# Kernel optimization log

Measured on AMD Instinct MI355X. Metric: run time of the kernel, lower is better.

The kernel has to match this reference:

```python
import jax, jax.numpy as jnp
import numpy as np

C = 1024   # n_embd = dim_att = dim_k = dim_v
H = 16     # n_head
K = 64     # k_head_size
V = 64     # v_head_size
DF = 2048  # dim_ffn = (2*C)//32*32
B = 4
T = 1024
N_LAYER = 24
LAYER_ID = 12


def setup_inputs() -> dict:
    key = jax.random.key(0)
    ks = jax.random.split(key, 8)
    r01 = LAYER_ID / (N_LAYER - 1)
    r10 = 1.0 - LAYER_ID / N_LAYER
    ddd = (jnp.arange(C, dtype=jnp.float32) / C)[None, None, :]
    maa_x = 1.0 - ddd ** r10
    maa_k = 1.0 - ddd ** r10
    maa_v = 1.0 - (ddd ** r10 + 0.3 * r01)
    maa_r = 1.0 - ddd ** (0.5 * r10)
    n = jnp.arange(C, dtype=jnp.float32)
    zigzag = ((jnp.arange(C) + 1) % 3 - 1).astype(jnp.float32) * 0.1
    u = (r01 * (1.0 - n / (C - 1)) + zigzag).reshape(H, K)
    # LoRA mats: torch init is zeros / uniform(-0.01,0.01); use small uniform for both
    # so the token-shift LoRA path is actually exercised.
    w1 = jax.random.uniform(ks[0], (C, 96), minval=-0.01, maxval=0.01)
    w2 = jax.random.uniform(ks[1], (3, 32, C), minval=-0.01, maxval=0.01)
    s = 0.02
    Wr = jax.random.normal(ks[2], (C, C)) * s
    Wk = jax.random.normal(ks[3], (C, C)) * s
    Wvg = jax.random.normal(ks[4], (C, 2 * (C + DF))) * s
    Wo = jax.random.normal(ks[5], (C + DF, C)) * s
    ln_g = jnp.ones((C,), jnp.float32)
    ln_b = jnp.zeros((C,), jnp.float32)
    x = jax.random.normal(ks[6], (B, T, C), dtype=jnp.float32)
    return dict(x=x, maa_x=maa_x, maa_k=maa_k, maa_v=maa_v, maa_r=maa_r,
                w1=w1, w2=w2, u=u, Wr=Wr, Wk=Wk, Wvg=Wvg, Wo=Wo,
                ln_g=ln_g, ln_b=ln_b)


def _wkv6(r, k, v, e, u):
    # r,k,e: (B,T,H,K); v: (B,T,H,V); u: (H,K). Decayed linear-attention scan.
    rt = r.transpose(1, 0, 2, 3)
    kt = k.transpose(1, 0, 2, 3)
    vt = v.transpose(1, 0, 2, 3)
    et = e.transpose(1, 0, 2, 3)

    def step(S, inp):  # S: (B,H,K,V)
        r_t, k_t, v_t, e_t = inp
        kv = k_t[..., :, None] * v_t[..., None, :]           # (B,H,K,V)
        out = jnp.einsum('bhk,bhkv->bhv', r_t, S + u[None, :, :, None] * kv)
        return S * e_t[..., :, None] + kv, out

    S0 = jnp.zeros((r.shape[0], u.shape[0], u.shape[1], v.shape[-1]), r.dtype)
    _, o = jax.lax.scan(step, S0, (rt, kt, vt, et))
    return o.transpose(1, 0, 2, 3)  # (B,T,H,V)


def reference(x, maa_x, maa_k, maa_v, maa_r, w1, w2, u, Wr, Wk, Wvg, Wo, ln_g, ln_b):
    Bx, Tx, Cx = x.shape
    # time_shift: ZeroPad2d((0,0,1,-1)) -> shift right by 1 along T with zero pad
    xs = jnp.concatenate([jnp.zeros_like(x[:, :1]), x[:, :-1]], axis=1)
    xx = xs - x
    xxx = x + xx * maa_x
    m = jnp.tanh(xxx @ w1).reshape(Bx, Tx, 3, -1)        # (B,T,3,32)
    m = jnp.einsum('btld,ldc->lbtc', m, w2)              # (3,B,T,C)
    mk, mv, mr = m[0], m[1], m[2]
    xk = x + xx * (maa_k + mk)
    xv = x + xx * (maa_v + mv)
    xr = x + xx * (maa_r + mr)
    r = xr @ Wr
    w = xk @ Wk
    e = jnp.exp(-jnp.exp(w))   # per-channel decay used by the WKV kernel
    k = 1.0 - e                # k = 1 - exp(-exp(w))
    vg = xv @ Wvg
    vffn, gate = jnp.split(vg, 2, axis=-1)
    vffn = vffn * jax.nn.silu(gate)
    v, ffn = vffn[..., :Cx], vffn[..., Cx:]
    o = _wkv6(r.reshape(Bx, Tx, H, K), k.reshape(Bx, Tx, H, K),
              v.reshape(Bx, Tx, H, V), e.reshape(Bx, Tx, H, K), u)
    o = o.reshape(Bx, Tx, Cx)
    mu = o.mean(-1, keepdims=True)
    var = o.var(-1, keepdims=True)
    o = (o - mu) / jnp.sqrt(var + 1e-5) * ln_g + ln_b
    return jnp.concatenate([o, ffn], axis=-1) @ Wo
```

## Files before the change

### kernel.cpp

```cpp
#include <hip/hip_runtime.h>
#include <hip/hip_bf16.h>
#include <math.h>

#define Bn 4
#define Tn 1024
#define Cn 1024
#define Hn 16
#define Kn 64
#define DFn 2048
#define NCn 16
#define Ln 64

typedef __bf16 bf16x8 __attribute__((ext_vector_type(8)));
typedef float f32x4 __attribute__((ext_vector_type(4)));

#define GLD(dst, src) \
  __builtin_amdgcn_global_load_lds((__attribute__((address_space(1))) const void*)(src), \
                                   (__attribute__((address_space(3))) void*)(dst), 16, 0, 0)

__device__ __forceinline__ float rdlane(float v, int l) {
  return __int_as_float(__builtin_amdgcn_readlane(__float_as_int(v), l));
}

__device__ __forceinline__ unsigned short bfbits(float f) {
  union { __hip_bfloat16 h; unsigned short u; } cv;
  cv.h = __float2bfloat16(f);
  return cv.u;
}

__global__ __launch_bounds__(256) void k_prep(const float* __restrict__ x,
                                              const float* __restrict__ maa_x,
                                              float* __restrict__ xx,
                                              __hip_bfloat16* __restrict__ xxx16) {
  int idx = blockIdx.x * 256 + threadIdx.x;
  int c4 = idx & 255;
  int bt = idx >> 8;
  int t = bt & (Tn - 1);
  const float4* x4 = (const float4*)x;
  float4 xv = x4[idx];
  float4 xp;
  if (t > 0) xp = x4[idx - 256];
  else { xp.x = 0.f; xp.y = 0.f; xp.z = 0.f; xp.w = 0.f; }
  float4 d;
  d.x = xp.x - xv.x; d.y = xp.y - xv.y; d.z = xp.z - xv.z; d.w = xp.w - xv.w;
  float4 m = ((const float4*)maa_x)[c4];
  ushort4 o;
  o.x = bfbits(fmaf(d.x, m.x, xv.x));
  o.y = bfbits(fmaf(d.y, m.y, xv.y));
  o.z = bfbits(fmaf(d.z, m.z, xv.z));
  o.w = bfbits(fmaf(d.w, m.w, xv.w));
  ((float4*)xx)[idx] = d;
  ((ushort4*)xxx16)[idx] = o;
}

__global__ __launch_bounds__(256) void k_mix1_16(const __hip_bfloat16* __restrict__ A,
                                                 const __hip_bfloat16* __restrict__ Bt,
                                                 __hip_bfloat16* __restrict__ m1) {
  const int K = 1024;
  __shared__ __align__(16) __hip_bfloat16 Al[128 * 32];
  __shared__ __align__(16) __hip_bfloat16 Bl[96 * 32];
  const int tid = threadIdx.x;
  const int wid = tid >> 6, lane = tid & 63;
  const int wr = wid >> 1, wc = wid & 1;
  const int row0 = blockIdx.x * 128;
  const char* gsrc[4];
  char* ldst[4];
  bool act[4];
  #pragma unroll
  for (int i = 0; i < 4; ++i) {
    const int s = i * 4 + wid;
    act[i] = (s < 14);
    const int ss = act[i] ? s : 0;
    if (ss < 8) {
      const int r = ss * 16 + (lane >> 2);
      gsrc[i] = (const char*)(A + (size_t)(row0 + r) * K) + (lane & 3) * 16;
      ldst[i] = (char*)&Al[0] + ss * 1024;
    } else {
      const int r = (ss - 8) * 16 + (lane >> 2);
      gsrc[i] = (const char*)(Bt + (size_t)r * K) + (lane & 3) * 16;
      ldst[i] = (char*)&Bl[0] + (ss - 8) * 1024;
    }
  }
  f32x4 acc[4][3];
  #pragma unroll
  for (int i = 0; i < 4; ++i)
    #pragma unroll
    for (int j = 0; j < 3; ++j)
      acc[i][j] = (f32x4){0.f, 0.f, 0.f, 0.f};
  const int g = lane >> 4, m = lane & 15;
  for (int k0 = 0; k0 < K; k0 += 32) {
    #pragma unroll
    for (int i = 0; i < 4; ++i) if (act[i]) GLD(ldst[i], gsrc[i]);
    #pragma unroll
    for (int i = 0; i < 4; ++i) gsrc[i] += 64;
    __syncthreads();
    bf16x8 af[4], bfr[3];
    #pragma unroll
    for (int i = 0; i < 4; ++i)
      af[i] = *(const bf16x8*)&Al[(wr * 64 + i * 16 + m) * 32 + g * 8];
    #pragma unroll
    for (int j = 0; j < 3; ++j)
      bfr[j] = *(const bf16x8*)&Bl[(wc * 48 + j * 16 + m) * 32 + g * 8];
    #pragma unroll
    for (int i = 0; i < 4; ++i)
      #pragma unroll
      for (int j = 0; j < 3; ++j)
        acc[i][j] = __builtin_amdgcn_mfma_f32_16x16x32_bf16(af[i], bfr[j], acc[i][j], 0, 0, 0);
    __syncthreads();
  }
  #pragma unroll
  for (int i = 0; i < 4; ++i) {
    const int grow = row0 + wr * 64 + i * 16 + g * 4;
    #pragma unroll
    for (int j = 0; j < 3; ++j) {
      const int gcol = wc * 48 + j * 16 + m;
      #pragma unroll
      for (int e = 0; e < 4; ++e)
        m1[(size_t)(grow + e) * 96 + gcol] = __float2bfloat16(tanhf(acc[i][j][e]));
    }
  }
}

__global__ __launch_bounds__(256) void k_mix2_16(const __hip_bfloat16* __restrict__ m1,
                                                 const __hip_bfloat16* __restrict__ w2t,
                                                 const float* __restrict__ x,
                                                 const float* __restrict__ xx,
                                                 const float* __restrict__ maa_k,
                                                 const float* __restrict__ maa_v,
                                                 const float* __restrict__ maa_r,
                                                 __hip_bfloat16* __restrict__ xk,
                                                 __hip_bfloat16* __restrict__ xv,
                                                 __hip_bfloat16* __restrict__ xr) {
  __shared__ __align__(16) __hip_bfloat16 Al[128 * 96];
  __shared__ __align__(16) __hip_bfloat16 Bl[3 * 64 * 32];
  const int tid = threadIdx.x;
  const int wid = tid >> 6, lane = tid & 63;
  const int wr = wid >> 1, wc = wid & 1;
  const int row0 = blockIdx.y * 128, col0 = blockIdx.x * 64;
  {
    const char* abase = (const char*)(m1 + (size_t)row0 * 96) + lane * 16;
    #pragma unroll
    for (int i = 0; i < 6; ++i) {
      const int s = wid + i * 4;
      GLD((char*)&Al[0] + s * 1024, abase + s * 1024);
    }
  }
  {
    const char* bbase = (const char*)w2t + (size_t)col0 * 64 + lane * 16;
    #pragma unroll
    for (int i = 0; i < 3; ++i) {
      const int s = wid + i * 4;
      const int l = s >> 2, q = s & 3;
      GLD((char*)&Bl[0] + s * 1024, bbase + (size_t)l * 65536 + q * 1024);
    }
  }
  __syncthreads();
  const int g = lane >> 4, m = lane & 15;
  f32x4 a0[4][2], a1[4][2], a2[4][2];
  #pragma unroll
  for (int i = 0; i < 4; ++i)
    #pragma unroll
    for (int j = 0; j < 2; ++j) {
      a0[i][j] = (f32x4){0.f,0.f,0.f,0.f};
      a1[i][j] = (f32x4){0.f,0.f,0.f,0.f};
      a2[i][j] = (f32x4){0.f,0.f,0.f,0.f};
    }
  #pragma unroll
  for (int l = 0; l < 3; ++l) {
    bf16x8 af[4], bfj[2];
    #pragma unroll
    for (int i = 0; i < 4; ++i)
      af[i] = *(const bf16x8*)&Al[(wr * 64 + i * 16 + m) * 96 + l * 32 + g * 8];
    #pragma unroll
    for (int j = 0; j < 2; ++j)
      bfj[j] = *(const bf16x8*)&Bl[(l * 64 + wc * 32 + j * 16 + m) * 32 + g * 8];
    #pragma unroll
    for (int i = 0; i < 4; ++i)
      #pragma unroll
      for (int j = 0; j < 2; ++j) {
        if (l == 0) a0[i][j] = __builtin_amdgcn_mfma_f32_16x16x32_bf16(af[i], bfj[j], a0[i][j], 0, 0, 0);
        if (l == 1) a1[i][j] = __builtin_amdgcn_mfma_f32_16x16x32_bf16(af[i], bfj[j], a1[i][j], 0, 0, 0);
        if (l == 2) a2[i][j] = __builtin_amdgcn_mfma_f32_16x16x32_bf16(af[i], bfj[j], a2[i][j], 0, 0, 0);
      }
  }
  #pragma unroll
  for (int i = 0; i < 4; ++i) {
    const int grow = row0 + wr * 64 + i * 16 + g * 4;
    #pragma unroll
    for (int j = 0; j < 2; ++j) {
      const int gcol = col0 + wc * 32 + j * 16 + m;
      const float mk_ = maa_k[gcol], mv_ = maa_v[gcol], mr_ = maa_r[gcol];
      #pragma unroll
      for (int e = 0; e < 4; ++e) {
        const size_t off = (size_t)(grow + e) * 1024 + gcol;
        const float xval = x[off], xxv = xx[off];
        xk[off] = __float2bfloat16(fmaf(xxv, mk_ + a0[i][j][e], xval));
        xv[off] = __float2bfloat16(fmaf(xxv, mv_ + a1[i][j][e], xval));
        xr[off] = __float2bfloat16(fmaf(xxv, mr_ + a2[i][j][e], xval));
      }
    }
  }
}

__global__ __launch_bounds__(256) void k_cvt_all(const float* __restrict__ w1,
                                                 const float* __restrict__ w2,
                                                 const float* __restrict__ Wr,
                                                 const float* __restrict__ Wk,
                                                 const float* __restrict__ Wvg,
                                                 const float* __restrict__ Wo,
                                                 __hip_bfloat16* __restrict__ w1t,
                                                 __hip_bfloat16* __restrict__ w2t,
                                                 __hip_bfloat16* __restrict__ Wrt,
                                                 __hip_bfloat16* __restrict__ Wkt,
                                                 __hip_bfloat16* __restrict__ Wvgt,
                                                 __hip_bfloat16* __restrict__ Wot) {
  int b = blockIdx.x;
  const float* W; __hip_bfloat16* Wt; int K, N, nx, rel;
  if (b < 96)        { W = w1;  Wt = w1t;  K = 1024; N = 96;   nx = 3;   rel = b; }
  else if (b < 192)  { int l = (b - 96) >> 5; rel = (b - 96) & 31;
                       W = w2 + l * 32768; Wt = w2t + l * 32768; K = 32; N = 1024; nx = 32; }
  else if (b < 1216) { W = Wr;  Wt = Wrt;  K = 1024; N = 1024; nx = 32;  rel = b - 192; }
  else if (b < 2240) { W = Wk;  Wt = Wkt;  K = 1024; N = 1024; nx = 32;  rel = b - 1216; }
  else if (b < 8384) { W = Wvg; Wt = Wvgt; K = 1024; N = 6144; nx = 192; rel = b - 2240; }
  else               { W = Wo;  Wt = Wot;  K = 3072; N = 1024; nx = 32;  rel = b - 8384; }
  int n0 = (rel % nx) * 32, k0 = (rel / nx) * 32;
  __shared__ float tile[32][33];
  int tid = threadIdx.x;
  int c = tid & 31, r = tid >> 5;
  #pragma unroll
  for (int i = 0; i < 4; ++i)
    tile[r + i * 8][c] = W[(size_t)(k0 + r + i * 8) * N + n0 + c];
  __syncthreads();
  #pragma unroll
  for (int i = 0; i < 4; ++i)
    Wt[(size_t)(n0 + r + i * 8) * K + k0 + c] = __float2bfloat16(tile[c][r + i * 8]);
}

template <int FN, int EPI>
__global__ __launch_bounds__(256) void k_gemm16(const __hip_bfloat16* __restrict__ A,
                                                const __hip_bfloat16* __restrict__ Bt,
                                                float* __restrict__ C,
                                                const int K, const int N) {
  constexpr int BN = FN * 32;
  constexpr int NISS = 8 + BN / 16;
  constexpr int PW = NISS / 4;
  __shared__ __align__(16) __hip_bfloat16 Al[128 * 32];
  __shared__ __align__(16) __hip_bfloat16 Bl[BN * 32];
  const int tid = threadIdx.x;
  const int wid = tid >> 6, lane = tid & 63;
  const int wr = wid >> 1, wc = wid & 1;
  const int row0 = blockIdx.y * 128, col0 = blockIdx.x * BN;
  const char* gsrc[PW];
  char* ldst[PW];
  #pragma unroll
  for (int i = 0; i < PW; ++i) {
    const int s = wid + i * 4;
    if (s < 8) {
      const int r = s * 16 + (lane >> 2);
      gsrc[i] = (const char*)(A + (size_t)(row0 + r) * K) + (lane & 3) * 16;
      ldst[i] = (char*)&Al[0] + s * 1024;
    } else {
      const int r = (s - 8) * 16 + (lane >> 2);
      gsrc[i] = (const char*)(Bt + (size_t)(col0 + r) * K) + (lane & 3) * 16;
      ldst[i] = (char*)&Bl[0] + (s - 8) * 1024;
    }
  }
  f32x4 acc[4][FN];
  #pragma unroll
  for (int i = 0; i < 4; ++i)
    #pragma unroll
    for (int j = 0; j < FN; ++j)
      acc[i][j] = (f32x4){0.f, 0.f, 0.f, 0.f};
  const int g = lane >> 4, m = lane & 15;
  for (int k0 = 0; k0 < K; k0 += 32) {
    #pragma unroll
    for (int i = 0; i < PW; ++i) GLD(ldst[i], gsrc[i]);
    #pragma unroll
    for (int i = 0; i < PW; ++i) gsrc[i] += 64;
    __syncthreads();
    bf16x8 af[4], bfr[FN];
    #pragma unroll
    for (int i = 0; i < 4; ++i)
      af[i] = *(const bf16x8*)&Al[(wr * 64 + i * 16 + m) * 32 + g * 8];
    #pragma unroll
    for (int j = 0; j < FN; ++j)
      bfr[j] = *(const bf16x8*)&Bl[(wc * (BN / 2) + j * 16 + m) * 32 + g * 8];
    #pragma unroll
    for (int i = 0; i < 4; ++i)
      #pragma unroll
      for (int j = 0; j < FN; ++j)
        acc[i][j] = __builtin_amdgcn_mfma_f32_16x16x32_bf16(af[i], bfr[j], acc[i][j], 0, 0, 0);
    __syncthreads();
  }
  #pragma unroll
  for (int i = 0; i < 4; ++i) {
    const int grow = row0 + wr * 64 + i * 16 + g * 4;
    #pragma unroll
    for (int j = 0; j < FN; ++j) {
      const int gcol = col0 + wc * (BN / 2) + j * 16 + m;
      #pragma unroll
      for (int e = 0; e < 4; ++e) {
        float val = acc[i][j][e];
        if (EPI == 1) val = expf(-expf(val));
        C[(size_t)(grow + e) * N + gcol] = val;
      }
    }
  }
}

__global__ __launch_bounds__(256) void k_gemm_vg16(const __hip_bfloat16* __restrict__ A,
                                                   const __hip_bfloat16* __restrict__ Bt,
                                                   float* __restrict__ v,
                                                   __hip_bfloat16* __restrict__ ffn) {
  const int K = 1024;
  __shared__ __align__(16) __hip_bfloat16 Al[128 * 32];
  __shared__ __align__(16) __hip_bfloat16 B1l[64 * 32];
  __shared__ __align__(16) __hip_bfloat16 B2l[64 * 32];
  const int tid = threadIdx.x;
  const int wid = tid >> 6, lane = tid & 63;
  const int wr = wid >> 1, wc = wid & 1;
  const int row0 = blockIdx.y * 128, col0 = blockIdx.x * 64;
  const char* gsrc[4];
  char* ldst[4];
  #pragma unroll
  for (int i = 0; i < 4; ++i) {
    const int s = wid + i * 4;
    if (s < 8) {
      const int r = s * 16 + (lane >> 2);
      gsrc[i] = (const char*)(A + (size_t)(row0 + r) * K) + (lane & 3) * 16;
      ldst[i] = (char*)&Al[0] + s * 1024;
    } else if (s < 12) {
      const int r = col0 + (s - 8) * 16 + (lane >> 2);
      gsrc[i] = (const char*)(Bt + (size_t)r * K) + (lane & 3) * 16;
      ldst[i] = (char*)&B1l[0] + (s - 8) * 1024;
    } else {
      const int r = 3072 + col0 + (s - 12) * 16 + (lane >> 2);
      gsrc[i] = (const char*)(Bt + (size_t)r * K) + (lane & 3) * 16;
      ldst[i] = (char*)&B2l[0] + (s - 12) * 1024;
    }
  }
  f32x4 a1[4][2], a2[4][2];
  #pragma unroll
  for (int i = 0; i < 4; ++i)
    #pragma unroll
    for (int j = 0; j < 2; ++j) {
      a1[i][j] = (f32x4){0.f, 0.f, 0.f, 0.f};
      a2[i][j] = (f32x4){0.f, 0.f, 0.f, 0.f};
    }
  const int g = lane >> 4, m = lane & 15;
  for (int k0 = 0; k0 < K; k0 += 32) {
    #pragma unroll
    for (int i = 0; i < 4; ++i) GLD(ldst[i], gsrc[i]);
    #pragma unroll
    for (int i = 0; i < 4; ++i) gsrc[i] += 64;
    __syncthreads();
    bf16x8 af[4], b1f[2], b2f[2];
    #pragma unroll
    for (int i = 0; i < 4; ++i)
      af[i] = *(const bf16x8*)&Al[(wr * 64 + i * 16 + m) * 32 + g * 8];
    #pragma unroll
    for (int j = 0; j < 2; ++j) {
      b1f[j] = *(const bf16x8*)&B1l[(wc * 32 + j * 16 + m) * 32 + g * 8];
      b2f[j] = *(const bf16x8*)&B2l[(wc * 32 + j * 16 + m) * 32 + g * 8];
    }
    #pragma unroll
    for (int i = 0; i < 4; ++i)
      #pragma unroll
      for (int j = 0; j < 2; ++j) {
        a1[i][j] = __builtin_amdgcn_mfma_f32_16x16x32_bf16(af[i], b1f[j], a1[i][j], 0, 0, 0);
        a2[i][j] = __builtin_amdgcn_mfma_f32_16x16x32_bf16(af[i], b2f[j], a2[i][j], 0, 0, 0);
      }
    __syncthreads();
  }
  const bool to_v = (col0 < 1024);
  #pragma unroll
  for (int i = 0; i < 4; ++i) {
    const int grow = row0 + wr * 64 + i * 16 + g * 4;
    #pragma unroll
    for (int j = 0; j < 2; ++j) {
      const int gcol = col0 + wc * 32 + j * 16 + m;
      #pragma unroll
      for (int e = 0; e < 4; ++e) {
        float gate = a2[i][j][e];
        float val = a1[i][j][e] * (gate / (1.f + expf(-gate)));
        if (to_v) v[(size_t)(grow + e) * 1024 + gcol] = val;
        else ffn[(size_t)(grow + e) * 2048 + (gcol - 1024)] = __float2bfloat16(val);
      }
    }
  }
}

__global__ __launch_bounds__(256) void k_gemm_wo16(const __hip_bfloat16* __restrict__ A1,
                                                   const __hip_bfloat16* __restrict__ A2,
                                                   const __hip_bfloat16* __restrict__ Bt,
                                                   float* __restrict__ C) {
  const int Kt = 3072;
  __shared__ __align__(16) __hip_bfloat16 Al[128 * 32];
  __shared__ __align__(16) __hip_bfloat16 Bl[64 * 32];
  const int tid = threadIdx.x;
  const int wid = tid >> 6, lane = tid & 63;
  const int wr = wid >> 1, wc = wid & 1;
  const int row0 = blockIdx.y * 128, col0 = blockIdx.x * 64;
  const char* gsrc[3];
  char* ldst[3];
  #pragma unroll
  for (int i = 0; i < 3; ++i) {
    const int s = wid + i * 4;
    if (s < 8) {
      const int r = s * 16 + (lane >> 2);
      gsrc[i] = (const char*)(A1 + (size_t)(row0 + r) * 1024) + (lane & 3) * 16;
      ldst[i] = (char*)&Al[0] + s * 1024;
    } else {
      const int r = col0 + (s - 8) * 16 + (lane >> 2);
      gsrc[i] = (const char*)(Bt + (size_t)r * Kt) + (lane & 3) * 16;
      ldst[i] = (char*)&Bl[0] + (s - 8) * 1024;
    }
  }
  f32x4 acc[4][2];
  #pragma unroll
  for (int i = 0; i < 4; ++i)
    #pragma unroll
    for (int j = 0; j < 2; ++j)
      acc[i][j] = (f32x4){0.f, 0.f, 0.f, 0.f};
  const int g = lane >> 4, m = lane & 15;

  #define WO_STEP() do {                                                          \
    _Pragma("unroll")                                                             \
    for (int i = 0; i < 3; ++i) GLD(ldst[i], gsrc[i]);                            \
    _Pragma("unroll")                                                             \
    for (int i = 0; i < 3; ++i) gsrc[i] += 64;                                    \
    __syncthreads();                                                              \
    bf16x8 af[4], bfr[2];                                                         \
    _Pragma("unroll")                                                             \
    for (int i = 0; i < 4; ++i)                                                   \
      af[i] = *(const bf16x8*)&Al[(wr * 64 + i * 16 + m) * 32 + g * 8];           \
    _Pragma("unroll")                                                             \
    for (int j = 0; j < 2; ++j)                                                   \
      bfr[j] = *(const bf16x8*)&Bl[(wc * 32 + j * 16 + m) * 32 + g * 8];          \
    _Pragma("unroll")                                                             \
    for (int i = 0; i < 4; ++i)                                                   \
      _Pragma("unroll")                                                           \
      for (int j = 0; j < 2; ++j)                                                 \
        acc[i][j] = __builtin_amdgcn_mfma_f32_16x16x32_bf16(af[i], bfr[j],        \
                                                            acc[i][j], 0, 0, 0); \
    __syncthreads();                                                              \
  } while (0)

  for (int k0 = 0; k0 < 1024; k0 += 32) WO_STEP();
  #pragma unroll
  for (int i = 0; i < 3; ++i) {
    const int s = wid + i * 4;
    if (s < 8) {
      const int r = s * 16 + (lane >> 2);
      gsrc[i] = (const char*)(A2 + (size_t)(row0 + r) * 2048) + (lane & 3) * 16;
    }
  }
  for (int k0 = 0; k0 < 2048; k0 += 32) WO_STEP();
  #undef WO_STEP

  #pragma unroll
  for (int i = 0; i < 4; ++i) {
    const int grow = row0 + wr * 64 + i * 16 + g * 4;
    #pragma unroll
    for (int j = 0; j < 2; ++j) {
      const int gcol = col0 + wc * 32 + j * 16 + m;
      #pragma unroll
      for (int e = 0; e < 4; ++e)
        C[(size_t)(grow + e) * 1024 + gcol] = acc[i][j][e];
    }
  }
}

#define TTn 8
__global__ __launch_bounds__(256) void k_wkv1(const float* __restrict__ r,
                                              const float* __restrict__ e,
                                              const float* __restrict__ v,
                                              const float* __restrict__ u,
                                              float* __restrict__ o,
                                              float* __restrict__ Dcum,
                                              float* __restrict__ Dtot,
                                              float* __restrict__ Inc) {
  int blk = blockIdx.x;
  int c = blk & (NCn - 1);
  int bh = blk >> 4;
  int b = bh >> 4, h = bh & 15;
  int tid = threadIdx.x, wave = tid >> 6, lane = tid & 63;
  size_t base = (size_t)b * Tn * Cn + (size_t)h * 64 + (size_t)c * Ln * Cn;
  int jbase = wave * 16 + (lane & 15);
  float uv = u[h * 64 + jbase];
  float st[16];
  #pragma unroll
  for (int i = 0; i < 16; ++i) st[i] = 0.f;
  float cum = 1.f;
  __shared__ float yp[4][TTn][64];
  for (int tb = 0; tb < Ln / TTn; ++tb) {
    float rv8[TTn], ev8[TTn], vv8[TTn];
    #pragma unroll
    for (int tt = 0; tt < TTn; ++tt) {
      size_t off = base + (size_t)(tb * TTn + tt) * Cn;
      rv8[tt] = r[off + jbase];
      ev8[tt] = e[off + jbase];
      vv8[tt] = v[off + lane];
    }
    float yb[TTn];
    #pragma unroll
    for (int tt = 0; tt < TTn; ++tt) {
      const float rv = rv8[tt], ev = ev8[tt], vv = vv8[tt];
      if (lane < 16)
        Dcum[base + (size_t)(tb * TTn + tt) * Cn + jbase] = cum;
      cum *= ev;
      float p = rv * uv * (1.f - ev);
      p += __shfl_xor(p, 1, 16);
      p += __shfl_xor(p, 2, 16);
      p += __shfl_xor(p, 4, 16);
      p += __shfl_xor(p, 8, 16);
      float y = p * vv;
      #pragma unroll
      for (int jj = 0; jj < 16; ++jj) {
        float rj = rdlane(rv, jj);
        float ej = rdlane(ev, jj);
        float kv = fmaf(-ej, vv, vv);
        y = fmaf(rj, st[jj], y);
        st[jj] = fmaf(st[jj], ej, kv);
      }
      yb[tt] = y;
    }
    #pragma unroll
    for (int tt = 0; tt < TTn; ++tt) yp[wave][tt][lane] = yb[tt];
    __syncthreads();
    #pragma unroll
    for (int q = 0; q < TTn / 4; ++q) {
      int tt = wave * (TTn / 4) + q;
      size_t off = base + (size_t)(tb * TTn + tt) * Cn;
      o[off + lane] = yp[0][tt][lane] + yp[1][tt][lane] + yp[2][tt][lane] + yp[3][tt][lane];
    }
    __syncthreads();
  }
  size_t sbase = ((size_t)bh * NCn + c) * 4096;
  #pragma unroll
  for (int jj = 0; jj < 16; ++jj)
    Inc[sbase + (size_t)(wave * 16 + jj) * 64 + lane] = st[jj];
  if (lane < 16)
    Dtot[((size_t)bh * NCn + c) * 64 + jbase] = cum;
}

__global__ __launch_bounds__(256) void k_wkv2(float* __restrict__ S,
                                              const float* __restrict__ Dtot) {
  int bh = blockIdx.x;
  int tid = threadIdx.x;
  float4 s[4];
  #pragma unroll
  for (int j = 0; j < 4; ++j) { s[j].x = 0.f; s[j].y = 0.f; s[j].z = 0.f; s[j].w = 0.f; }
  size_t sb = (size_t)bh * NCn * 4096;
  for (int c = 0; c < NCn; ++c) {
    float4* entry = (float4*)(S + sb + (size_t)c * 4096);
    const float* dt = Dtot + ((size_t)bh * NCn + c) * 64;
    #pragma unroll
    for (int j = 0; j < 4; ++j) {
      int idx4 = tid + j * 256;
      int k = idx4 >> 4;
      float d = dt[k];
      float4 inc = entry[idx4];
      float4 cur = s[j];
      entry[idx4] = cur;
      s[j].x = fmaf(cur.x, d, inc.x);
      s[j].y = fmaf(cur.y, d, inc.y);
      s[j].z = fmaf(cur.z, d, inc.z);
      s[j].w = fmaf(cur.w, d, inc.w);
    }
  }
}

__global__ __launch_bounds__(256) void k_wkv3(const float* __restrict__ r,
                                              const float* __restrict__ Dcum,
                                              const float* __restrict__ S,
                                              float* __restrict__ o) {
  int blk = blockIdx.x;
  int c = blk & (NCn - 1);
  if (c == 0) return;
  int bh = blk >> 4;
  int b = bh >> 4, h = bh & 15;
  int tid = threadIdx.x, wave = tid >> 6, lane = tid & 63;
  const float* Sg = S + ((size_t)bh * NCn + c) * 4096;
  float sreg[64];
  #pragma unroll
  for (int k = 0; k < 64; ++k) sreg[k] = Sg[k * 64 + lane];
  size_t base = (size_t)b * Tn * Cn + (size_t)h * 64 + (size_t)c * Ln * Cn;
  for (int ti = 0; ti < 16; ++ti) {
    int t = wave * 16 + ti;
    size_t off = base + (size_t)t * Cn;
    float rd = r[off + lane] * Dcum[off + lane];
    float y = 0.f;
    #pragma unroll
    for (int k = 0; k < 64; ++k)
      y = fmaf(rdlane(rd, k), sreg[k], y);
    o[off + lane] += y;
  }
}

__global__ __launch_bounds__(256) void k_ln(const float* __restrict__ o,
                                            const float* __restrict__ g,
                                            const float* __restrict__ bta,
                                            __hip_bfloat16* __restrict__ ln16) {
  int bt = blockIdx.x, tid = threadIdx.x;
  const float4* row = (const float4*)(o + (size_t)bt * 1024);
  float4 v = row[tid];
  float s = v.x + v.y + v.z + v.w;
  float s2 = fmaf(v.x, v.x, fmaf(v.y, v.y, fmaf(v.z, v.z, v.w * v.w)));
  #pragma unroll
  for (int m = 1; m < 64; m <<= 1) {
    s += __shfl_xor(s, m, 64);
    s2 += __shfl_xor(s2, m, 64);
  }
  __shared__ float rs[4], rq[4];
  if ((tid & 63) == 0) { rs[tid >> 6] = s; rq[tid >> 6] = s2; }
  __syncthreads();
  s = rs[0] + rs[1] + rs[2] + rs[3];
  s2 = rq[0] + rq[1] + rq[2] + rq[3];
  float mu = s * (1.f / 1024.f);
  float var = s2 * (1.f / 1024.f) - mu * mu;
  float rstd = rsqrtf(var + 1e-5f);
  float4 gv = ((const float4*)g)[tid];
  float4 bv = ((const float4*)bta)[tid];
  ushort4 outv;
  outv.x = bfbits(fmaf((v.x - mu) * rstd, gv.x, bv.x));
  outv.y = bfbits(fmaf((v.y - mu) * rstd, gv.y, bv.y));
  outv.z = bfbits(fmaf((v.z - mu) * rstd, gv.z, bv.z));
  outv.w = bfbits(fmaf((v.w - mu) * rstd, gv.w, bv.w));
  ((ushort4*)((unsigned short*)ln16 + (size_t)bt * 1024))[tid] = outv;
}

extern "C" void kernel_launch(void* const* d_in, const int* in_sizes, int n_in,
                              void* d_out, int out_size, void* d_ws, size_t ws_size,
                              hipStream_t stream) {
  const float* x     = (const float*)d_in[0];
  const float* maa_x = (const float*)d_in[1];
  const float* maa_k = (const float*)d_in[2];
  const float* maa_v = (const float*)d_in[3];
  const float* maa_r = (const float*)d_in[4];
  const float* w1    = (const float*)d_in[5];
  const float* w2    = (const float*)d_in[6];
  const float* u     = (const float*)d_in[7];
  const float* Wr    = (const float*)d_in[8];
  const float* Wk    = (const float*)d_in[9];
  const float* Wvg   = (const float*)d_in[10];
  const float* Wo    = (const float*)d_in[11];
  const float* ln_g  = (const float*)d_in[12];
  const float* ln_b  = (const float*)d_in[13];
  float* out = (float*)d_out;
  float* ws = (float*)d_ws;

  const size_t M1 = 1048576;
  float* xx    = ws;
  __hip_bfloat16* xxx16 = (__hip_bfloat16*)(ws + 4 * M1);
  __hip_bfloat16* m1_16 = (__hip_bfloat16*)(ws + 8 * M1);
  __hip_bfloat16* w1t = (__hip_bfloat16*)(ws + 8 * M1 + 393216);
  __hip_bfloat16* w2t = (__hip_bfloat16*)(ws + 8 * M1 + 442368);
  __hip_bfloat16* xk16 = (__hip_bfloat16*)(ws + 8 * M1 + 524288);
  __hip_bfloat16* xv16 = (__hip_bfloat16*)(ws + 10 * M1 + 524288);
  __hip_bfloat16* xr16 = (__hip_bfloat16*)(ws + 12 * M1 + 524288);
  float* ee    = ws + 14 * M1 + 524288;
  float* vv    = ws + 18 * M1 + 524288;
  float* Sbuf  = ws + 22 * M1 + 524288;
  __hip_bfloat16* ffn16 = (__hip_bfloat16*)(ws + 26 * M1 + 524288);
  __hip_bfloat16* Wr16t = (__hip_bfloat16*)(ws + 30 * M1 + 524288);
  __hip_bfloat16* Wk16t = (__hip_bfloat16*)(ws + 31 * M1);
  __hip_bfloat16* Wvg16t = (__hip_bfloat16*)(ws + 31 * M1 + 524288);
  __hip_bfloat16* Wo16t = (__hip_bfloat16*)(ws + 34 * M1 + 524288);
  float* rr = ws + 4 * M1;
  float* oo = xx;
  float* Dcum = ws + 8 * M1 + 524288;
  float* Dtot = (float*)m1_16;
  __hip_bfloat16* ln16 = (__hip_bfloat16*)Sbuf;

  k_cvt_all<<<11456, 256, 0, stream>>>(w1, w2, Wr, Wk, Wvg, Wo,
                                       w1t, w2t, Wr16t, Wk16t, Wvg16t, Wo16t);

  k_prep<<<4096, 256, 0, stream>>>(x, maa_x, xx, xxx16);
  k_mix1_16<<<32, 256, 0, stream>>>(xxx16, w1t, m1_16);
  k_mix2_16<<<dim3(16, 32), 256, 0, stream>>>(m1_16, w2t, x, xx, maa_k, maa_v, maa_r,
                                              xk16, xv16, xr16);
  k_gemm16<2, 0><<<dim3(16, 32), 256, 0, stream>>>(xr16, Wr16t, rr, 1024, 1024);
  k_gemm_vg16<<<dim3(48, 32), 256, 0, stream>>>(xv16, Wvg16t, vv, ffn16);
  k_gemm16<2, 1><<<dim3(16, 32), 256, 0, stream>>>(xk16, Wk16t, ee, 1024, 1024);
  k_wkv1<<<64 * NCn, 256, 0, stream>>>(rr, ee, vv, u, oo, Dcum, Dtot, Sbuf);
  k_wkv2<<<64, 256, 0, stream>>>(Sbuf, Dtot);
  k_wkv3<<<64 * NCn, 256, 0, stream>>>(rr, Dcum, Sbuf, oo);
  k_ln<<<4096, 256, 0, stream>>>(oo, ln_g, ln_b, ln16);
  k_gemm_wo16<<<dim3(16, 32), 256, 0, stream>>>(ln16, ffn16, Wo16t, out);
}
```

Measured before the change: 339.0 us.

## Merge Wr/Wk GEMMs into one launch and widen VG GEMM tile to 128 columns

The r and k projection GEMMs are combined into a single kernel launch that uses blockIdx.z to pick the operands and whether to apply the exp(-exp) epilogue. This removes one launch and gives a larger grid of 1024 blocks. The fused value/gate GEMM now uses 128-column tiles instead of 64, so each A tile is reused across twice as many outputs and the grid drops to 768 blocks. The trade-off is more accumulator registers (64 f32x4) and more LDS per block, which may lower occupancy.

```diff
diff --git a/kernel.cpp b/kernel.cpp
--- a/kernel.cpp
+++ b/kernel.cpp
@@ -236,24 +236,27 @@
     Wt[(size_t)(n0 + r + i * 8) * K + k0 + c] = __float2bfloat16(tile[c][r + i * 8]);
 }
 
-template <int FN, int EPI>
-__global__ __launch_bounds__(256) void k_gemm16(const __hip_bfloat16* __restrict__ A,
-                                                const __hip_bfloat16* __restrict__ Bt,
-                                                float* __restrict__ C,
-                                                const int K, const int N) {
-  constexpr int BN = FN * 32;
-  constexpr int NISS = 8 + BN / 16;
-  constexpr int PW = NISS / 4;
+__global__ __launch_bounds__(256) void k_gemm_re(const __hip_bfloat16* __restrict__ Ar,
+                                                 const __hip_bfloat16* __restrict__ Btr,
+                                                 float* __restrict__ Cr,
+                                                 const __hip_bfloat16* __restrict__ Ak,
+                                                 const __hip_bfloat16* __restrict__ Btk,
+                                                 float* __restrict__ Ck) {
+  const int K = 1024, N = 1024;
+  const int z = blockIdx.z;
+  const __hip_bfloat16* A  = z ? Ak : Ar;
+  const __hip_bfloat16* Bt = z ? Btk : Btr;
+  float* C = z ? Ck : Cr;
   __shared__ __align__(16) __hip_bfloat16 Al[128 * 32];
-  __shared__ __align__(16) __hip_bfloat16 Bl[BN * 32];
+  __shared__ __align__(16) __hip_bfloat16 Bl[64 * 32];
   const int tid = threadIdx.x;
   const int wid = tid >> 6, lane = tid & 63;
   const int wr = wid >> 1, wc = wid & 1;
-  const int row0 = blockIdx.y * 128, col0 = blockIdx.x * BN;
-  const char* gsrc[PW];
-  char* ldst[PW];
-  #pragma unroll
-  for (int i = 0; i < PW; ++i) {
+  const int row0 = blockIdx.y * 128, col0 = blockIdx.x * 64;
+  const char* gsrc[3];
+  char* ldst[3];
+  #pragma unroll
+  for (int i = 0; i < 3; ++i) {
     const int s = wid + i * 4;
     if (s < 8) {
       const int r = s * 16 + (lane >> 2);
@@ -265,30 +268,30 @@
       ldst[i] = (char*)&Bl[0] + (s - 8) * 1024;
     }
   }
-  f32x4 acc[4][FN];
+  f32x4 acc[4][2];
   #pragma unroll
   for (int i = 0; i < 4; ++i)
     #pragma unroll
-    for (int j = 0; j < FN; ++j)
+    for (int j = 0; j < 2; ++j)
       acc[i][j] = (f32x4){0.f, 0.f, 0.f, 0.f};
   const int g = lane >> 4, m = lane & 15;
   for (int k0 = 0; k0 < K; k0 += 32) {
     #pragma unroll
-    for (int i = 0; i < PW; ++i) GLD(ldst[i], gsrc[i]);
-    #pragma unroll
-    for (int i = 0; i < PW; ++i) gsrc[i] += 64;
-    __syncthreads();
-    bf16x8 af[4], bfr[FN];
+    for (int i = 0; i < 3; ++i) GLD(ldst[i], gsrc[i]);
+    #pragma unroll
+    for (int i = 0; i < 3; ++i) gsrc[i] += 64;
+    __syncthreads();
+    bf16x8 af[4], bfr[2];
     #pragma unroll
     for (int i = 0; i < 4; ++i)
       af[i] = *(const bf16x8*)&Al[(wr * 64 + i * 16 + m) * 32 + g * 8];
     #pragma unroll
-    for (int j = 0; j < FN; ++j)
-      bfr[j] = *(const bf16x8*)&Bl[(wc * (BN / 2) + j * 16 + m) * 32 + g * 8];
-    #pragma unroll
-    for (int i = 0; i < 4; ++i)
-      #pragma unroll
-      for (int j = 0; j < FN; ++j)
+    for (int j = 0; j < 2; ++j)
+      bfr[j] = *(const bf16x8*)&Bl[(wc * 32 + j * 16 + m) * 32 + g * 8];
+    #pragma unroll
+    for (int i = 0; i < 4; ++i)
+      #pragma unroll
+      for (int j = 0; j < 2; ++j)
         acc[i][j] = __builtin_amdgcn_mfma_f32_16x16x32_bf16(af[i], bfr[j], acc[i][j], 0, 0, 0);
     __syncthreads();
   }
@@ -296,12 +299,12 @@
   for (int i = 0; i < 4; ++i) {
     const int grow = row0 + wr * 64 + i * 16 + g * 4;
     #pragma unroll
-    for (int j = 0; j < FN; ++j) {
-      const int gcol = col0 + wc * (BN / 2) + j * 16 + m;
+    for (int j = 0; j < 2; ++j) {
+      const int gcol = col0 + wc * 32 + j * 16 + m;
       #pragma unroll
       for (int e = 0; e < 4; ++e) {
         float val = acc[i][j][e];
-        if (EPI == 1) val = expf(-expf(val));
+        if (z) val = expf(-expf(val));
         C[(size_t)(grow + e) * N + gcol] = val;
       }
     }
@@ -314,59 +317,59 @@
                                                    __hip_bfloat16* __restrict__ ffn) {
   const int K = 1024;
   __shared__ __align__(16) __hip_bfloat16 Al[128 * 32];
-  __shared__ __align__(16) __hip_bfloat16 B1l[64 * 32];
-  __shared__ __align__(16) __hip_bfloat16 B2l[64 * 32];
+  __shared__ __align__(16) __hip_bfloat16 B1l[128 * 32];
+  __shared__ __align__(16) __hip_bfloat16 B2l[128 * 32];
   const int tid = threadIdx.x;
   const int wid = tid >> 6, lane = tid & 63;
   const int wr = wid >> 1, wc = wid & 1;
-  const int row0 = blockIdx.y * 128, col0 = blockIdx.x * 64;
-  const char* gsrc[4];
-  char* ldst[4];
-  #pragma unroll
-  for (int i = 0; i < 4; ++i) {
+  const int row0 = blockIdx.y * 128, col0 = blockIdx.x * 128;
+  const char* gsrc[6];
+  char* ldst[6];
+  #pragma unroll
+  for (int i = 0; i < 6; ++i) {
     const int s = wid + i * 4;
     if (s < 8) {
       const int r = s * 16 + (lane >> 2);
       gsrc[i] = (const char*)(A + (size_t)(row0 + r) * K) + (lane & 3) * 16;
       ldst[i] = (char*)&Al[0] + s * 1024;
-    } else if (s < 12) {
+    } else if (s < 16) {
       const int r = col0 + (s - 8) * 16 + (lane >> 2);
       gsrc[i] = (const char*)(Bt + (size_t)r * K) + (lane & 3) * 16;
       ldst[i] = (char*)&B1l[0] + (s - 8) * 1024;
     } else {
-      const int r = 3072 + col0 + (s - 12) * 16 + (lane >> 2);
+      const int r = 3072 + col0 + (s - 16) * 16 + (lane >> 2);
       gsrc[i] = (const char*)(Bt + (size_t)r * K) + (lane & 3) * 16;
-      ldst[i] = (char*)&B2l[0] + (s - 12) * 1024;
-    }
-  }
-  f32x4 a1[4][2], a2[4][2];
+      ldst[i] = (char*)&B2l[0] + (s - 16) * 1024;
+    }
+  }
+  f32x4 a1[4][4], a2[4][4];
   #pragma unroll
   for (int i = 0; i < 4; ++i)
     #pragma unroll
-    for (int j = 0; j < 2; ++j) {
+    for (int j = 0; j < 4; ++j) {
       a1[i][j] = (f32x4){0.f, 0.f, 0.f, 0.f};
       a2[i][j] = (f32x4){0.f, 0.f, 0.f, 0.f};
     }
   const int g = lane >> 4, m = lane & 15;
   for (int k0 = 0; k0 < K; k0 += 32) {
     #pragma unroll
-    for (int i = 0; i < 4; ++i) GLD(ldst[i], gsrc[i]);
-    #pragma unroll
-    for (int i = 0; i < 4; ++i) gsrc[i] += 64;
-    __syncthreads();
-    bf16x8 af[4], b1f[2], b2f[2];
+    for (int i = 0; i < 6; ++i) GLD(ldst[i], gsrc[i]);
+    #pragma unroll
+    for (int i = 0; i < 6; ++i) gsrc[i] += 64;
+    __syncthreads();
+    bf16x8 af[4], b1f[4], b2f[4];
     #pragma unroll
     for (int i = 0; i < 4; ++i)
       af[i] = *(const bf16x8*)&Al[(wr * 64 + i * 16 + m) * 32 + g * 8];
     #pragma unroll
-    for (int j = 0; j < 2; ++j) {
-      b1f[j] = *(const bf16x8*)&B1l[(wc * 32 + j * 16 + m) * 32 + g * 8];
-      b2f[j] = *(const bf16x8*)&B2l[(wc * 32 + j * 16 + m) * 32 + g * 8];
-    }
-    #pragma unroll
-    for (int i = 0; i < 4; ++i)
-      #pragma unroll
-      for (int j = 0; j < 2; ++j) {
+    for (int j = 0; j < 4; ++j) {
+      b1f[j] = *(const bf16x8*)&B1l[(wc * 64 + j * 16 + m) * 32 + g * 8];
+      b2f[j] = *(const bf16x8*)&B2l[(wc * 64 + j * 16 + m) * 32 + g * 8];
+    }
+    #pragma unroll
+    for (int i = 0; i < 4; ++i)
+      #pragma unroll
+      for (int j = 0; j < 4; ++j) {
         a1[i][j] = __builtin_amdgcn_mfma_f32_16x16x32_bf16(af[i], b1f[j], a1[i][j], 0, 0, 0);
         a2[i][j] = __builtin_amdgcn_mfma_f32_16x16x32_bf16(af[i], b2f[j], a2[i][j], 0, 0, 0);
       }
@@ -377,8 +380,8 @@
   for (int i = 0; i < 4; ++i) {
     const int grow = row0 + wr * 64 + i * 16 + g * 4;
     #pragma unroll
-    for (int j = 0; j < 2; ++j) {
-      const int gcol = col0 + wc * 32 + j * 16 + m;
+    for (int j = 0; j < 4; ++j) {
+      const int gcol = col0 + wc * 64 + j * 16 + m;
       #pragma unroll
       for (int e = 0; e < 4; ++e) {
         float gate = a2[i][j][e];
@@ -680,9 +683,8 @@
   k_mix1_16<<<32, 256, 0, stream>>>(xxx16, w1t, m1_16);
   k_mix2_16<<<dim3(16, 32), 256, 0, stream>>>(m1_16, w2t, x, xx, maa_k, maa_v, maa_r,
                                               xk16, xv16, xr16);
-  k_gemm16<2, 0><<<dim3(16, 32), 256, 0, stream>>>(xr16, Wr16t, rr, 1024, 1024);
-  k_gemm_vg16<<<dim3(48, 32), 256, 0, stream>>>(xv16, Wvg16t, vv, ffn16);
-  k_gemm16<2, 1><<<dim3(16, 32), 256, 0, stream>>>(xk16, Wk16t, ee, 1024, 1024);
+  k_gemm_re<<<dim3(16, 32, 2), 256, 0, stream>>>(xr16, Wr16t, rr, xk16, Wk16t, ee);
+  k_gemm_vg16<<<dim3(24, 32), 256, 0, stream>>>(xv16, Wvg16t, vv, ffn16);
   k_wkv1<<<64 * NCn, 256, 0, stream>>>(rr, ee, vv, u, oo, Dcum, Dtot, Sbuf);
   k_wkv2<<<64, 256, 0, stream>>>(Sbuf, Dtot);
   k_wkv3<<<64 * NCn, 256, 0, stream>>>(rr, Dcum, Sbuf, oo);
```

Result: slower. 380.8 us (+12.3%).
